# Kernel tuning notes

Hardware: AMD Instinct MI355X
Metric: run time of the kernel (lower is better)

The kernel has to match this reference:

```python
import jax, jax.numpy as jnp
import numpy as np
from jax import lax

# Cl(3,0) Cayley table: W_eff[i, j] = sum_k T[i, j, k] * w[k], signs transcribed
# verbatim from the 64 scatter ops in _cl300_expand_batched.
_TABLE = [
    [(0, 0, 1), (1, 1, 1), (2, 2, 1), (3, 3, 1), (4, 4, -1), (5, 5, -1), (6, 6, -1), (7, 7, -1)],
    [(1, 0, 1), (0, 1, 1), (4, 2, -1), (5, 3, -1), (2, 4, 1), (3, 5, 1), (7, 6, -1), (6, 7, -1)],
    [(2, 0, 1), (4, 1, 1), (0, 2, 1), (6, 3, -1), (1, 4, -1), (7, 5, 1), (3, 6, 1), (5, 7, 1)],
    [(3, 0, 1), (5, 1, 1), (6, 2, 1), (0, 3, 1), (7, 4, -1), (1, 5, -1), (2, 6, -1), (4, 7, -1)],
    [(4, 0, 1), (2, 1, 1), (1, 2, -1), (7, 3, 1), (0, 4, 1), (6, 5, -1), (5, 6, 1), (3, 7, 1)],
    [(5, 0, 1), (3, 1, 1), (7, 2, -1), (1, 3, -1), (6, 4, 1), (0, 5, 1), (4, 6, -1), (2, 7, -1)],
    [(6, 0, 1), (7, 1, 1), (3, 2, 1), (2, 3, -1), (5, 4, -1), (4, 5, 1), (0, 6, 1), (1, 7, 1)],
    [(7, 0, 1), (6, 1, 1), (5, 2, -1), (4, 3, 1), (3, 4, 1), (2, 5, -1), (1, 6, 1), (0, 7, 1)],
]

def _cayley():
    T = np.zeros((8, 8, 8), np.float32)
    for i, row in enumerate(_TABLE):
        for j, k, s in row:
            T[i, j, k] = s
    return jnp.asarray(T)


def setup_inputs() -> dict:
    key = jax.random.key(0)
    k0, k1 = jax.random.split(key, 2)
    B, F, P, G = 16, 8, 4, 32
    state = jax.random.normal(k0, (B, F, 8, G, G, G), jnp.float32)
    all_weights = jax.random.normal(k1, (F, P, 27, 8), jnp.float32) * 0.05
    # mimic _init_weights: zero the center tap, identity-ish on pass 0
    all_weights = all_weights.at[:, :, 26, :].set(0.0).at[:, 0, 26, 0].set(0.8)
    all_biases = jnp.zeros((F, P, 8), jnp.float32)
    field_mix_logits = jnp.tile(jnp.eye(F, dtype=jnp.float32) * 3.0, (P, 1, 1))
    pass_alpha_logit = jnp.full((P,), -1.0, jnp.float32)
    gate_weight = jnp.full((F, 8), 0.1, jnp.float32)
    gate_bias = jnp.full((F, 8), 2.0, jnp.float32)
    return dict(state=state, all_weights=all_weights, all_biases=all_biases,
                field_mix_logits=field_mix_logits, pass_alpha_logit=pass_alpha_logit,
                gate_weight=gate_weight, gate_bias=gate_bias)


def reference(state, all_weights, all_biases, field_mix_logits,
              pass_alpha_logit, gate_weight, gate_bias):
    B, F, _, G, _, _ = state.shape
    P = all_weights.shape[1]
    G3 = G * G * G
    T = _cayley()
    # sparse signed Cayley expansion: [F,P,27,8] -> [F,P,8,8,3,3,3]
    W_eff = jnp.einsum('ijk,fpck->fpijc', T, all_weights).reshape(F, P, 8, 8, 3, 3, 3)
    mix_all = jax.nn.softmax(field_mix_logits, axis=2)  # [P,F,F]
    x = state
    old_state = state
    for p in range(P):
        x_before = x
        Wg = W_eff[:, p].reshape(F * 8, 8, 3, 3, 3)
        bg = all_biases[:, p].reshape(F * 8)
        xf = x.reshape(B, F * 8, G, G, G)
        # causal shifted conv: asymmetric pad (2,0) per spatial dim, grouped by field
        y = lax.conv_general_dilated(
            xf, Wg, window_strides=(1, 1, 1), padding=[(2, 0), (2, 0), (2, 0)],
            dimension_numbers=('NCDHW', 'OIDHW', 'NCDHW'), feature_group_count=F)
        y = jnp.tanh(y + bg[None, :, None, None, None])  # [B,F*8,G,G,G]
        # cross-field mixing (bmm with shared mix matrix)
        xm = jnp.einsum('gf,bfm->bgm', mix_all[p], y.reshape(B, F, 8 * G3))
        x = xm.reshape(B, F, 8, G, G, G)
        alpha = jax.nn.sigmoid(pass_alpha_logit[p])
        x = alpha * x_before + (1.0 - alpha) * x
    gw = gate_weight.reshape(1, F, 8, 1, 1, 1)
    gb = gate_bias.reshape(1, F, 8, 1, 1, 1)
    gate = jax.nn.sigmoid(gw * old_state + gb)
    return gate * old_state + (1.0 - gate) * x
```

## Files before the change

### kernel.cpp

```cpp
#include <hip/hip_runtime.h>
#include <math.h>

#define B_  16
#define F_  8
#define C_  8
#define G_  32
#define G3_ 32768
#define P_  4
#define N_  (B_*F_*C_*G3_)
#define SF_ (C_*G3_)
#define SB_ (F_*SF_)
#define APACK_SZ (P_*F_*9*64*8)

typedef __attribute__((ext_vector_type(8))) short short8v;
typedef __attribute__((ext_vector_type(4))) float f32x4;
typedef unsigned short u16;
typedef unsigned int u32;

__device__ __constant__ int c_k[8][8] = {
  {0,1,2,3,4,5,6,7},
  {1,0,4,5,2,3,7,6},
  {2,4,0,6,1,7,3,5},
  {3,5,6,0,7,1,2,4},
  {4,2,1,7,0,6,5,3},
  {5,3,7,1,6,0,4,2},
  {6,7,3,2,5,4,0,1},
  {7,6,5,4,3,2,1,0}};
__device__ __constant__ float c_s[8][8] = {
  { 1, 1, 1, 1,-1,-1,-1,-1},
  { 1, 1, 1, 1,-1,-1,-1,-1},
  { 1,-1, 1, 1, 1, 1,-1, 1},
  { 1,-1,-1, 1,-1, 1, 1,-1},
  { 1,-1, 1, 1, 1, 1,-1, 1},
  { 1,-1,-1, 1,-1, 1, 1,-1},
  { 1, 1,-1, 1, 1,-1, 1, 1},
  { 1, 1,-1, 1, 1,-1, 1, 1}};

__device__ __forceinline__ float fast_tanh(float v) {
  float e = __expf(2.f * v);
  return 1.f - 2.f / (e + 1.f);
}
__device__ __forceinline__ float fast_sig(float v) {
  return 1.f / (1.f + __expf(-v));
}
__device__ __forceinline__ u32 bf16_rne(float v) {
  u32 u = __float_as_uint(v);
  return (u + 0x7FFFu + ((u >> 16) & 1u)) >> 16;
}
__device__ __forceinline__ u32 pk_bf16(float a, float b) {
  u32 d;
  asm("v_cvt_pk_bf16_f32 %0, %1, %2" : "=v"(d) : "v"(a), "v"(b));
  return d;
}
__device__ __forceinline__ float bl(u32 u) { return __uint_as_float(u << 16); }
__device__ __forceinline__ float bh(u32 u) { return __uint_as_float(u & 0xffff0000u); }
__device__ __forceinline__ float b16f(u16 v) { return __uint_as_float(((u32)v) << 16); }

#define HS(pt) (((pt) + ((pt) >> 2)) & 3)

__global__ void prep_kernel(const float* __restrict__ all_weights,
                            const float* __restrict__ mix_logits,
                            u16* __restrict__ Apack,
                            float* __restrict__ mix) {
  int idx = blockIdx.x * 256 + threadIdx.x;
  if (idx < APACK_SZ) {
    int e = idx & 7;
    int l = (idx >> 3) & 63;
    int rest = idx >> 9;
    int t = rest % 9;
    int fp = rest / 9;
    int f = fp & 7, p = fp >> 3;
    int g = l >> 4, m = l & 15;
    int zoff = m >> 3, i = m & 7;
    int kk = g*4 + (e & 3) + ((e >= 4) ? 16 : 0);
    int zl = kk >> 3, j = kk & 7;
    int dz = zl - zoff;
    float val = 0.f;
    if (dz >= 0 && dz <= 2)
      val = c_s[i][j] * all_weights[((f*P_ + p)*27 + (dz*9 + t))*8 + c_k[i][j]];
    Apack[idx] = (u16)bf16_rne(val);
  }
  if (blockIdx.x == 0 && threadIdx.x < P_*F_) {
    int p = threadIdx.x / F_, g = threadIdx.x % F_;
    const float* row = &mix_logits[(p*F_ + g)*F_];
    float mx = row[0];
    for (int f = 1; f < F_; ++f) mx = fmaxf(mx, row[f]);
    float e[F_]; float sum = 0.f;
    for (int f = 0; f < F_; ++f) { e[f] = __expf(row[f] - mx); sum += e[f]; }
    float inv = 1.f / sum;
    for (int f = 0; f < F_; ++f) mix[(p*F_ + g)*F_ + f] = e[f] * inv;
  }
}

#define RSTG 6
#define TPTS 204

template<int MODE>
__device__ __forceinline__ uint4 field_step(
    int f, const void* __restrict__ xsrc_, const u16* __restrict__ Apack,
    const float* __restrict__ biases, int p, int b, int z0, int y0,
    u32* xk, int tid, int lane, int wid, int g, int ln) {
  if (f) __syncthreads();

  if (tid < 192) {
    int qq  = tid / 48;
    int r2  = tid - qq*48;
    int row = r2 >> 3;
    int c   = r2 & 7;
    int zl = qq >> 1, jq = qq & 1;
    int gz0 = z0 - 2 + zl;
    int gy  = y0 - 2 + row;
    int gx  = c * 4;
    int off = (jq*4)*G3_ + gz0*1024 + gy*32 + gx;
    int ptb = row*34 + 2 + gx;
    u32 d0[4], d1[4], d2[4], d3[4];
    if (MODE != 0) {
      const u16* s0 = (const u16*)xsrc_ + (size_t)b*SB_ + f*SF_ + off;
      const u16* s1 = s0 + 2048;
      uint2 a0={0,0},a1={0,0},a2={0,0},a3={0,0};
      uint2 e0={0,0},e1={0,0},e2={0,0},e3={0,0};
      if (gy >= 0) {
        if (gz0 >= 0) {
          a0 = *(const uint2*)(s0);
          a1 = *(const uint2*)(s0 + G3_);
          a2 = *(const uint2*)(s0 + 2*G3_);
          a3 = *(const uint2*)(s0 + 3*G3_);
        }
        e0 = *(const uint2*)(s1);
        e1 = *(const uint2*)(s1 + G3_);
        e2 = *(const uint2*)(s1 + 2*G3_);
        e3 = *(const uint2*)(s1 + 3*G3_);
      }
      d0[0] = __builtin_amdgcn_perm(a1.x, a0.x, 0x05040100u);
      d0[1] = __builtin_amdgcn_perm(a1.x, a0.x, 0x07060302u);
      d0[2] = __builtin_amdgcn_perm(a1.y, a0.y, 0x05040100u);
      d0[3] = __builtin_amdgcn_perm(a1.y, a0.y, 0x07060302u);
      d1[0] = __builtin_amdgcn_perm(a3.x, a2.x, 0x05040100u);
      d1[1] = __builtin_amdgcn_perm(a3.x, a2.x, 0x07060302u);
      d1[2] = __builtin_amdgcn_perm(a3.y, a2.y, 0x05040100u);
      d1[3] = __builtin_amdgcn_perm(a3.y, a2.y, 0x07060302u);
      d2[0] = __builtin_amdgcn_perm(e1.x, e0.x, 0x05040100u);
      d2[1] = __builtin_amdgcn_perm(e1.x, e0.x, 0x07060302u);
      d2[2] = __builtin_amdgcn_perm(e1.y, e0.y, 0x05040100u);
      d2[3] = __builtin_amdgcn_perm(e1.y, e0.y, 0x07060302u);
      d3[0] = __builtin_amdgcn_perm(e3.x, e2.x, 0x05040100u);
      d3[1] = __builtin_amdgcn_perm(e3.x, e2.x, 0x07060302u);
      d3[2] = __builtin_amdgcn_perm(e3.y, e2.y, 0x05040100u);
      d3[3] = __builtin_amdgcn_perm(e3.y, e2.y, 0x07060302u);
    } else {
      const float* s0 = (const float*)xsrc_ + (size_t)b*SB_ + f*SF_ + off;
      const float* s1 = s0 + 2048;
      float4 A0={0,0,0,0},A1={0,0,0,0},A2={0,0,0,0},A3={0,0,0,0};
      float4 B0={0,0,0,0},B1={0,0,0,0},B2={0,0,0,0},B3={0,0,0,0};
      if (gy >= 0) {
        if (gz0 >= 0) {
          A0 = *(const float4*)(s0);
          A1 = *(const float4*)(s0 + G3_);
          A2 = *(const float4*)(s0 + 2*G3_);
          A3 = *(const float4*)(s0 + 3*G3_);
        }
        B0 = *(const float4*)(s1);
        B1 = *(const float4*)(s1 + G3_);
        B2 = *(const float4*)(s1 + 2*G3_);
        B3 = *(const float4*)(s1 + 3*G3_);
      }
      d0[0]=pk_bf16(A0.x,A1.x); d1[0]=pk_bf16(A2.x,A3.x);
      d2[0]=pk_bf16(B0.x,B1.x); d3[0]=pk_bf16(B2.x,B3.x);
      d0[1]=pk_bf16(A0.y,A1.y); d1[1]=pk_bf16(A2.y,A3.y);
      d2[1]=pk_bf16(B0.y,B1.y); d3[1]=pk_bf16(B2.y,B3.y);
      d0[2]=pk_bf16(A0.z,A1.z); d1[2]=pk_bf16(A2.z,A3.z);
      d2[2]=pk_bf16(B0.z,B1.z); d3[2]=pk_bf16(B2.z,B3.z);
      d0[3]=pk_bf16(A0.w,A1.w); d1[3]=pk_bf16(A2.w,A3.w);
      d2[3]=pk_bf16(B0.w,B1.w); d3[3]=pk_bf16(B2.w,B3.w);
    }
    #define STW(px) { \
      uint4 d; d.x = d0[px]; d.y = d1[px]; d.z = d2[px]; d.w = d3[px]; \
      int pt = ptb + px; \
      *(uint4*)&xk[pt*16 + ((qq ^ HS(pt)) << 2)] = d; }
    STW(0) STW(1) STW(2) STW(3)
    #undef STW
  }

  short8v a[9];
  const u16* ap = Apack + (size_t)((p*8 + f) * 9) * 512;
  #pragma unroll
  for (int t = 0; t < 9; ++t)
    a[t] = *(const short8v*)(ap + (t*64 + lane)*8);

  __syncthreads();

  f32x4 acc0 = {0.f,0.f,0.f,0.f}, acc1 = {0.f,0.f,0.f,0.f};
  #pragma unroll
  for (int dy = 0; dy < 3; ++dy) {
    int prow = (wid + dy)*34;
    #pragma unroll
    for (int dx = 0; dx < 3; ++dx) {
      int t = dy*3 + dx;
      int pt0 = prow + ln + dx;
      int dwb = pt0*16 + ((g ^ HS(pt0)) << 2);
      short8v b0 = *(const short8v*)&xk[dwb];
      short8v b1 = *(const short8v*)&xk[dwb + 256];
      acc0 = __builtin_amdgcn_mfma_f32_16x16x32_bf16(a[t], b0, acc0, 0, 0, 0);
      acc1 = __builtin_amdgcn_mfma_f32_16x16x32_bf16(a[t], b1, acc1, 0, 0, 0);
    }
  }

  const float* bb = biases + (f*P_ + p)*8 + (g & 1)*4;
  float b0v = bb[0], b1v = bb[1], b2v = bb[2], b3v = bb[3];
  uint4 yp;
  yp.x = pk_bf16(fast_tanh(acc0[0] + b0v), fast_tanh(acc0[1] + b1v));
  yp.y = pk_bf16(fast_tanh(acc0[2] + b2v), fast_tanh(acc0[3] + b3v));
  yp.z = pk_bf16(fast_tanh(acc1[0] + b0v), fast_tanh(acc1[1] + b1v));
  yp.w = pk_bf16(fast_tanh(acc1[2] + b2v), fast_tanh(acc1[3] + b3v));
  return yp;
}

template<int MODE>
__global__ __launch_bounds__(256, 4)
void fused_kernel(const void* __restrict__ xsrc_,
                  void* __restrict__ xdst_,
                  const float* __restrict__ state,
                  const u16* __restrict__ Apack,
                  const float* __restrict__ biases,
                  const float* __restrict__ mixb,
                  const float* __restrict__ pal,
                  const float* __restrict__ gw,
                  const float* __restrict__ gb,
                  int p) {
  __shared__ __align__(16) u32 xk[TPTS * 16];

  int bid = blockIdx.x;
  int yt = bid & 7;
  int zt = (bid >> 3) & 15;
  int b  =  bid >> 7;
  int z0 = zt * 2, y0 = yt * 4;
  int tid  = threadIdx.x;
  int lane = tid & 63;
  int wid  = tid >> 6;
  int g    = lane >> 4;
  int ln   = lane & 15;

  if (tid < 192) {
    int pt = (tid >> 5) * 34 + ((tid >> 4) & 1);
    xk[pt*16 + (tid & 15)] = 0u;
  }

  uint4 yp0 = field_step<MODE>(0, xsrc_, Apack, biases, p, b, z0, y0, xk, tid, lane, wid, g, ln);
  uint4 yp1 = field_step<MODE>(1, xsrc_, Apack, biases, p, b, z0, y0, xk, tid, lane, wid, g, ln);
  uint4 yp2 = field_step<MODE>(2, xsrc_, Apack, biases, p, b, z0, y0, xk, tid, lane, wid, g, ln);
  uint4 yp3 = field_step<MODE>(3, xsrc_, Apack, biases, p, b, z0, y0, xk, tid, lane, wid, g, ln);
  uint4 yp4 = field_step<MODE>(4, xsrc_, Apack, biases, p, b, z0, y0, xk, tid, lane, wid, g, ln);
  uint4 yp5 = field_step<MODE>(5, xsrc_, Apack, biases, p, b, z0, y0, xk, tid, lane, wid, g, ln);
  uint4 yp6 = field_step<MODE>(6, xsrc_, Apack, biases, p, b, z0, y0, xk, tid, lane, wid, g, ln);
  uint4 yp7 = field_step<MODE>(7, xsrc_, Apack, biases, p, b, z0, y0, xk, tid, lane, wid, g, ln);

  float yf[8][8];
  #define UNP(F, YPV) \
    yf[F][0]=bl(YPV.x); yf[F][1]=bh(YPV.x); yf[F][2]=bl(YPV.y); yf[F][3]=bh(YPV.y); \
    yf[F][4]=bl(YPV.z); yf[F][5]=bh(YPV.z); yf[F][6]=bl(YPV.w); yf[F][7]=bh(YPV.w);
  UNP(0,yp0) UNP(1,yp1) UNP(2,yp2) UNP(3,yp3)
  UNP(4,yp4) UNP(5,yp5) UNP(6,yp6) UNP(7,yp7)
  #undef UNP

  float alpha = fast_sig(pal[p]);
  float na = 1.f - alpha;
  int zoff = g >> 1;
  int i0 = (g & 1)*4;
  size_t ebase = (size_t)b*SB_ + (size_t)(z0 + zoff)*1024 + (size_t)(y0 + wid)*32 + ln;

  #pragma unroll
  for (int gg = 0; gg < 8; ++gg) {
    const float* mr = mixb + (p*8 + gg)*8;
    float o[8] = {0.f,0.f,0.f,0.f,0.f,0.f,0.f,0.f};
    #pragma unroll
    for (int f = 0; f < 8; ++f) {
      float m = mr[f];
      #pragma unroll
      for (int e = 0; e < 8; ++e) o[e] = fmaf(m, yf[f][e], o[e]);
    }
    size_t obase = ebase + (size_t)gg*SF_;
    #pragma unroll
    for (int e = 0; e < 8; ++e) {
      size_t idx = obase + (size_t)(i0 + (e & 3))*G3_ + (e >> 2)*16;
      float xbv;
      if (MODE == 0) xbv = ((const float*)xsrc_)[idx];
      else           xbv = b16f(((const u16*)xsrc_)[idx]);
      float xf = alpha*xbv + na*o[e];
      if (MODE == 2) {
        float st = state[idx];
        float w = gw[gg*8 + i0 + (e & 3)];
        float bbv = gb[gg*8 + i0 + (e & 3)];
        float gt = fast_sig(w*st + bbv);
        ((float*)xdst_)[idx] = gt*st + (1.f - gt)*xf;
      } else {
        ((u16*)xdst_)[idx] = (u16)bf16_rne(xf);
      }
    }
  }
}

extern "C" void kernel_launch(void* const* d_in, const int* in_sizes, int n_in,
                              void* d_out, int out_size, void* d_ws, size_t ws_size,
                              hipStream_t stream) {
  (void)in_sizes; (void)n_in; (void)out_size; (void)ws_size;
  const float* state       = (const float*)d_in[0];
  const float* all_weights = (const float*)d_in[1];
  const float* all_biases  = (const float*)d_in[2];
  const float* mix_logits  = (const float*)d_in[3];
  const float* pal         = (const float*)d_in[4];
  const float* gw          = (const float*)d_in[5];
  const float* gb          = (const float*)d_in[6];
  float* out = (float*)d_out;

  u16* X0 = (u16*)d_ws;
  u16* X1 = X0 + N_;
  u16* Apack = X1 + N_;
  float* mixb = (float*)(Apack + APACK_SZ);

  prep_kernel<<<dim3(APACK_SZ/256), dim3(256), 0, stream>>>(
      all_weights, mix_logits, Apack, mixb);

  dim3 grid(2048), blk(256);
  fused_kernel<0><<<grid, blk, 0, stream>>>((const void*)state, (void*)X0, state,
      Apack, all_biases, mixb, pal, gw, gb, 0);
  fused_kernel<1><<<grid, blk, 0, stream>>>((const void*)X0, (void*)X1, state,
      Apack, all_biases, mixb, pal, gw, gb, 1);
  fused_kernel<1><<<grid, blk, 0, stream>>>((const void*)X1, (void*)X0, state,
      Apack, all_biases, mixb, pal, gw, gb, 2);
  fused_kernel<2><<<grid, blk, 0, stream>>>((const void*)X0, (void*)out, state,
      Apack, all_biases, mixb, pal, gw, gb, 3);
}
```

Measured before the change: 320.8 us.

## Store intermediate bf16 state channel-interleaved for vector loads and stores

The intermediate bf16 state buffers switch from planar NCDHW layout to a point-major layout with the 8 Clifford channels of a field packed into one 16-byte word. The halo staging in shared memory becomes a single uint4 load per point with no byte permutes, and the epilogue reads and writes 8-byte packed pairs instead of scattered 2-byte elements. The weight packing in the prep kernel is reindexed to match the new K ordering, and the launch bound occupancy hint rises from 4 to 6 blocks per CU. The higher occupancy hint may force register spills.

```diff
diff --git a/kernel.cpp b/kernel.cpp
--- a/kernel.cpp
+++ b/kernel.cpp
@@ -54,7 +54,6 @@
 }
 __device__ __forceinline__ float bl(u32 u) { return __uint_as_float(u << 16); }
 __device__ __forceinline__ float bh(u32 u) { return __uint_as_float(u & 0xffff0000u); }
-__device__ __forceinline__ float b16f(u16 v) { return __uint_as_float(((u32)v) << 16); }
 
 #define HS(pt) (((pt) + ((pt) >> 2)) & 3)
 
@@ -64,7 +63,7 @@
                             float* __restrict__ mix) {
   int idx = blockIdx.x * 256 + threadIdx.x;
   if (idx < APACK_SZ) {
-    int e = idx & 7;
+    int j = idx & 7;
     int l = (idx >> 3) & 63;
     int rest = idx >> 9;
     int t = rest % 9;
@@ -72,9 +71,7 @@
     int f = fp & 7, p = fp >> 3;
     int g = l >> 4, m = l & 15;
     int zoff = m >> 3, i = m & 7;
-    int kk = g*4 + (e & 3) + ((e >= 4) ? 16 : 0);
-    int zl = kk >> 3, j = kk & 7;
-    int dz = zl - zoff;
+    int dz = g - zoff;
     float val = 0.f;
     if (dz >= 0 && dz <= 2)
       val = c_s[i][j] * all_weights[((f*P_ + p)*27 + (dz*9 + t))*8 + c_k[i][j]];
@@ -92,7 +89,6 @@
   }
 }
 
-#define RSTG 6
 #define TPTS 204
 
 template<int MODE>
@@ -102,82 +98,52 @@
     u32* xk, int tid, int lane, int wid, int g, int ln) {
   if (f) __syncthreads();
 
-  if (tid < 192) {
-    int qq  = tid / 48;
-    int r2  = tid - qq*48;
+  if (MODE != 0) {
+    const uint4* xp = (const uint4*)xsrc_ + (size_t)(b*8 + f)*G3_;
+    #pragma unroll
+    for (int it0 = 0; it0 < 3; ++it0) {
+      int it = it0*256 + tid;
+      int gx = it & 31;
+      int pr = it >> 5;
+      int zl = pr / 6;
+      int row = pr - zl*6;
+      int gz = z0 - 2 + zl;
+      int gy = y0 - 2 + row;
+      uint4 v = {0u,0u,0u,0u};
+      if (gz >= 0 && gy >= 0)
+        v = xp[gz*1024 + gy*32 + gx];
+      int pt = row*34 + 2 + gx;
+      *(uint4*)&xk[pt*16 + ((zl ^ HS(pt)) << 2)] = v;
+    }
+  } else if (tid < 192) {
+    int zl  = tid / 48;
+    int r2  = tid - zl*48;
     int row = r2 >> 3;
     int c   = r2 & 7;
-    int zl = qq >> 1, jq = qq & 1;
-    int gz0 = z0 - 2 + zl;
-    int gy  = y0 - 2 + row;
-    int gx  = c * 4;
-    int off = (jq*4)*G3_ + gz0*1024 + gy*32 + gx;
+    int gz = z0 - 2 + zl;
+    int gy = y0 - 2 + row;
+    int gx = c * 4;
+    const float* s0 = (const float*)xsrc_ + (size_t)b*SB_ + f*SF_
+                    + gz*1024 + gy*32 + gx;
+    float4 f0={0,0,0,0},f1={0,0,0,0},f2={0,0,0,0},f3={0,0,0,0};
+    float4 f4={0,0,0,0},f5={0,0,0,0},f6={0,0,0,0},f7={0,0,0,0};
+    if (gz >= 0 && gy >= 0) {
+      f0 = *(const float4*)(s0);
+      f1 = *(const float4*)(s0 + G3_);
+      f2 = *(const float4*)(s0 + 2*G3_);
+      f3 = *(const float4*)(s0 + 3*G3_);
+      f4 = *(const float4*)(s0 + 4*G3_);
+      f5 = *(const float4*)(s0 + 5*G3_);
+      f6 = *(const float4*)(s0 + 6*G3_);
+      f7 = *(const float4*)(s0 + 7*G3_);
+    }
     int ptb = row*34 + 2 + gx;
-    u32 d0[4], d1[4], d2[4], d3[4];
-    if (MODE != 0) {
-      const u16* s0 = (const u16*)xsrc_ + (size_t)b*SB_ + f*SF_ + off;
-      const u16* s1 = s0 + 2048;
-      uint2 a0={0,0},a1={0,0},a2={0,0},a3={0,0};
-      uint2 e0={0,0},e1={0,0},e2={0,0},e3={0,0};
-      if (gy >= 0) {
-        if (gz0 >= 0) {
-          a0 = *(const uint2*)(s0);
-          a1 = *(const uint2*)(s0 + G3_);
-          a2 = *(const uint2*)(s0 + 2*G3_);
-          a3 = *(const uint2*)(s0 + 3*G3_);
-        }
-        e0 = *(const uint2*)(s1);
-        e1 = *(const uint2*)(s1 + G3_);
-        e2 = *(const uint2*)(s1 + 2*G3_);
-        e3 = *(const uint2*)(s1 + 3*G3_);
-      }
-      d0[0] = __builtin_amdgcn_perm(a1.x, a0.x, 0x05040100u);
-      d0[1] = __builtin_amdgcn_perm(a1.x, a0.x, 0x07060302u);
-      d0[2] = __builtin_amdgcn_perm(a1.y, a0.y, 0x05040100u);
-      d0[3] = __builtin_amdgcn_perm(a1.y, a0.y, 0x07060302u);
-      d1[0] = __builtin_amdgcn_perm(a3.x, a2.x, 0x05040100u);
-      d1[1] = __builtin_amdgcn_perm(a3.x, a2.x, 0x07060302u);
-      d1[2] = __builtin_amdgcn_perm(a3.y, a2.y, 0x05040100u);
-      d1[3] = __builtin_amdgcn_perm(a3.y, a2.y, 0x07060302u);
-      d2[0] = __builtin_amdgcn_perm(e1.x, e0.x, 0x05040100u);
-      d2[1] = __builtin_amdgcn_perm(e1.x, e0.x, 0x07060302u);
-      d2[2] = __builtin_amdgcn_perm(e1.y, e0.y, 0x05040100u);
-      d2[3] = __builtin_amdgcn_perm(e1.y, e0.y, 0x07060302u);
-      d3[0] = __builtin_amdgcn_perm(e3.x, e2.x, 0x05040100u);
-      d3[1] = __builtin_amdgcn_perm(e3.x, e2.x, 0x07060302u);
-      d3[2] = __builtin_amdgcn_perm(e3.y, e2.y, 0x05040100u);
-      d3[3] = __builtin_amdgcn_perm(e3.y, e2.y, 0x07060302u);
-    } else {
-      const float* s0 = (const float*)xsrc_ + (size_t)b*SB_ + f*SF_ + off;
-      const float* s1 = s0 + 2048;
-      float4 A0={0,0,0,0},A1={0,0,0,0},A2={0,0,0,0},A3={0,0,0,0};
-      float4 B0={0,0,0,0},B1={0,0,0,0},B2={0,0,0,0},B3={0,0,0,0};
-      if (gy >= 0) {
-        if (gz0 >= 0) {
-          A0 = *(const float4*)(s0);
-          A1 = *(const float4*)(s0 + G3_);
-          A2 = *(const float4*)(s0 + 2*G3_);
-          A3 = *(const float4*)(s0 + 3*G3_);
-        }
-        B0 = *(const float4*)(s1);
-        B1 = *(const float4*)(s1 + G3_);
-        B2 = *(const float4*)(s1 + 2*G3_);
-        B3 = *(const float4*)(s1 + 3*G3_);
-      }
-      d0[0]=pk_bf16(A0.x,A1.x); d1[0]=pk_bf16(A2.x,A3.x);
-      d2[0]=pk_bf16(B0.x,B1.x); d3[0]=pk_bf16(B2.x,B3.x);
-      d0[1]=pk_bf16(A0.y,A1.y); d1[1]=pk_bf16(A2.y,A3.y);
-      d2[1]=pk_bf16(B0.y,B1.y); d3[1]=pk_bf16(B2.y,B3.y);
-      d0[2]=pk_bf16(A0.z,A1.z); d1[2]=pk_bf16(A2.z,A3.z);
-      d2[2]=pk_bf16(B0.z,B1.z); d3[2]=pk_bf16(B2.z,B3.z);
-      d0[3]=pk_bf16(A0.w,A1.w); d1[3]=pk_bf16(A2.w,A3.w);
-      d2[3]=pk_bf16(B0.w,B1.w); d3[3]=pk_bf16(B2.w,B3.w);
-    }
-    #define STW(px) { \
-      uint4 d; d.x = d0[px]; d.y = d1[px]; d.z = d2[px]; d.w = d3[px]; \
+    #define STW(px, CC) { \
+      uint4 d; d.x = pk_bf16(f0.CC, f1.CC); d.y = pk_bf16(f2.CC, f3.CC); \
+      d.z = pk_bf16(f4.CC, f5.CC); d.w = pk_bf16(f6.CC, f7.CC); \
       int pt = ptb + px; \
-      *(uint4*)&xk[pt*16 + ((qq ^ HS(pt)) << 2)] = d; }
-    STW(0) STW(1) STW(2) STW(3)
+      *(uint4*)&xk[pt*16 + ((zl ^ HS(pt)) << 2)] = d; }
+    STW(0, x) STW(1, y) STW(2, z) STW(3, w)
     #undef STW
   }
 
@@ -216,7 +182,7 @@
 }
 
 template<int MODE>
-__global__ __launch_bounds__(256, 4)
+__global__ __launch_bounds__(256, 6)
 void fused_kernel(const void* __restrict__ xsrc_,
                   void* __restrict__ xdst_,
                   const float* __restrict__ state,
@@ -266,7 +232,10 @@
   float na = 1.f - alpha;
   int zoff = g >> 1;
   int i0 = (g & 1)*4;
-  size_t ebase = (size_t)b*SB_ + (size_t)(z0 + zoff)*1024 + (size_t)(y0 + wid)*32 + ln;
+  size_t pt0 = (size_t)(b*8)*G3_ + (size_t)(z0 + zoff)*1024
+             + (size_t)(y0 + wid)*32 + ln;
+  size_t ebase = (size_t)b*SB_ + (size_t)(z0 + zoff)*1024
+               + (size_t)(y0 + wid)*32 + ln;
 
   #pragma unroll
   for (int gg = 0; gg < 8; ++gg) {
@@ -278,23 +247,42 @@
       #pragma unroll
       for (int e = 0; e < 8; ++e) o[e] = fmaf(m, yf[f][e], o[e]);
     }
-    size_t obase = ebase + (size_t)gg*SF_;
-    #pragma unroll
-    for (int e = 0; e < 8; ++e) {
-      size_t idx = obase + (size_t)(i0 + (e & 3))*G3_ + (e >> 2)*16;
-      float xbv;
-      if (MODE == 0) xbv = ((const float*)xsrc_)[idx];
-      else           xbv = b16f(((const u16*)xsrc_)[idx]);
-      float xf = alpha*xbv + na*o[e];
-      if (MODE == 2) {
+    size_t ptg = pt0 + (size_t)gg*G3_;
+    size_t og  = ebase + (size_t)gg*SF_;
+
+    float xb[8];
+    if (MODE == 0) {
+      #pragma unroll
+      for (int e = 0; e < 8; ++e)
+        xb[e] = ((const float*)xsrc_)[og + (size_t)(i0 + (e & 3))*G3_ + (e >> 2)*16];
+    } else {
+      const uint2* xbp = (const uint2*)xsrc_;
+      uint2 u0 = xbp[ptg*2 + (g & 1)];
+      uint2 u1 = xbp[(ptg + 16)*2 + (g & 1)];
+      xb[0]=bl(u0.x); xb[1]=bh(u0.x); xb[2]=bl(u0.y); xb[3]=bh(u0.y);
+      xb[4]=bl(u1.x); xb[5]=bh(u1.x); xb[6]=bl(u1.y); xb[7]=bh(u1.y);
+    }
+
+    if (MODE == 2) {
+      #pragma unroll
+      for (int e = 0; e < 8; ++e) {
+        size_t idx = og + (size_t)(i0 + (e & 3))*G3_ + (e >> 2)*16;
+        float xf = alpha*xb[e] + na*o[e];
         float st = state[idx];
-        float w = gw[gg*8 + i0 + (e & 3)];
-        float bbv = gb[gg*8 + i0 + (e & 3)];
-        float gt = fast_sig(w*st + bbv);
+        float w  = gw[gg*8 + i0 + (e & 3)];
+        float bv = gb[gg*8 + i0 + (e & 3)];
+        float gt = fast_sig(w*st + bv);
         ((float*)xdst_)[idx] = gt*st + (1.f - gt)*xf;
-      } else {
-        ((u16*)xdst_)[idx] = (u16)bf16_rne(xf);
       }
+    } else {
+      uint2* xdp = (uint2*)xdst_;
+      uint2 w0, w1;
+      w0.x = pk_bf16(alpha*xb[0] + na*o[0], alpha*xb[1] + na*o[1]);
+      w0.y = pk_bf16(alpha*xb[2] + na*o[2], alpha*xb[3] + na*o[3]);
+      w1.x = pk_bf16(alpha*xb[4] + na*o[4], alpha*xb[5] + na*o[5]);
+      w1.y = pk_bf16(alpha*xb[6] + na*o[6], alpha*xb[7] + na*o[7]);
+      xdp[ptg*2 + (g & 1)]        = w0;
+      xdp[(ptg + 16)*2 + (g & 1)] = w1;
     }
   }
 }
```

New measurement: 593.0 us. +84.8%, slower.

## Stage epilogue stores through LDS for vectorized writes, remap block order, raise occupancy

Applied to the files above, without the earlier changes.

The epilogue now writes each wave's mixed outputs into a per-wave shared-memory buffer and then emits wide 16-byte global stores, instead of scattered 2- or 4-byte stores per element. Block indices are remapped so consecutive blocks differ in y-tile stride, which changes L2 locality and the order in which CUs work through the tiles. The minimum-blocks hint in launch bounds goes from 4 to 6, which tightens the register budget and may cause spills. The extra LDS buffer adds shared-memory use per block, and the new ordering may help or hurt halo reuse.

```diff
diff --git a/kernel.cpp b/kernel.cpp
--- a/kernel.cpp
+++ b/kernel.cpp
@@ -92,7 +92,6 @@
   }
 }
 
-#define RSTG 6
 #define TPTS 204
 
 template<int MODE>
@@ -216,7 +215,7 @@
 }
 
 template<int MODE>
-__global__ __launch_bounds__(256, 4)
+__global__ __launch_bounds__(256, 6)
 void fused_kernel(const void* __restrict__ xsrc_,
                   void* __restrict__ xdst_,
                   const float* __restrict__ state,
@@ -228,8 +227,10 @@
                   const float* __restrict__ gb,
                   int p) {
   __shared__ __align__(16) u32 xk[TPTS * 16];
-
-  int bid = blockIdx.x;
+  __shared__ __align__(16) u32 obuf[4][576];
+
+  int orig = blockIdx.x;
+  int bid  = (orig & 7) * 256 + (orig >> 3);
   int yt = bid & 7;
   int zt = (bid >> 3) & 15;
   int b  =  bid >> 7;
@@ -268,6 +269,14 @@
   int i0 = (g & 1)*4;
   size_t ebase = (size_t)b*SB_ + (size_t)(z0 + zoff)*1024 + (size_t)(y0 + wid)*32 + ln;
 
+  u16*   ob16 = (u16*)&obuf[wid][0];
+  float* ob32 = (float*)&obuf[wid][0];
+  int srow = lane >> 2;
+  int sc   = srow >> 1, sz = srow & 1;
+  int sx   = (lane & 3) * 8;
+  size_t sbase = (size_t)b*SB_ + (size_t)sc*G3_ + (size_t)(z0 + sz)*1024
+               + (size_t)(y0 + wid)*32 + sx;
+
   #pragma unroll
   for (int gg = 0; gg < 8; ++gg) {
     const float* mr = mixb + (p*8 + gg)*8;
@@ -278,23 +287,43 @@
       #pragma unroll
       for (int e = 0; e < 8; ++e) o[e] = fmaf(m, yf[f][e], o[e]);
     }
-    size_t obase = ebase + (size_t)gg*SF_;
-    #pragma unroll
-    for (int e = 0; e < 8; ++e) {
-      size_t idx = obase + (size_t)(i0 + (e & 3))*G3_ + (e >> 2)*16;
-      float xbv;
-      if (MODE == 0) xbv = ((const float*)xsrc_)[idx];
-      else           xbv = b16f(((const u16*)xsrc_)[idx]);
-      float xf = alpha*xbv + na*o[e];
-      if (MODE == 2) {
+    size_t og = ebase + (size_t)gg*SF_;
+
+    float xb[8];
+    if (MODE == 0) {
+      #pragma unroll
+      for (int e = 0; e < 8; ++e)
+        xb[e] = ((const float*)xsrc_)[og + (size_t)(i0 + (e & 3))*G3_ + ((e >> 2) << 4)];
+    } else {
+      #pragma unroll
+      for (int e = 0; e < 8; ++e)
+        xb[e] = b16f(((const u16*)xsrc_)[og + (size_t)(i0 + (e & 3))*G3_ + ((e >> 2) << 4)]);
+    }
+
+    if (MODE == 2) {
+      #pragma unroll
+      for (int e = 0; e < 8; ++e) {
+        size_t idx = og + (size_t)(i0 + (e & 3))*G3_ + ((e >> 2) << 4);
+        float xf = alpha*xb[e] + na*o[e];
         float st = state[idx];
-        float w = gw[gg*8 + i0 + (e & 3)];
-        float bbv = gb[gg*8 + i0 + (e & 3)];
-        float gt = fast_sig(w*st + bbv);
-        ((float*)xdst_)[idx] = gt*st + (1.f - gt)*xf;
-      } else {
-        ((u16*)xdst_)[idx] = (u16)bf16_rne(xf);
+        float w  = gw[gg*8 + i0 + (e & 3)];
+        float bv = gb[gg*8 + i0 + (e & 3)];
+        float gt = fast_sig(w*st + bv);
+        ob32[((i0 + (e & 3))*2 + zoff)*36 + ln + ((e >> 2) << 4)] = gt*st + (1.f - gt)*xf;
       }
+      float4 v0 = *(const float4*)&ob32[srow*36 + sx];
+      float4 v1 = *(const float4*)&ob32[srow*36 + sx + 4];
+      float* op = (float*)xdst_ + sbase + (size_t)gg*SF_;
+      *(float4*)(op)     = v0;
+      *(float4*)(op + 4) = v1;
+    } else {
+      #pragma unroll
+      for (int e = 0; e < 8; ++e) {
+        float xf = alpha*xb[e] + na*o[e];
+        ob16[((i0 + (e & 3))*2 + zoff)*32 + ln + ((e >> 2) << 4)] = (u16)bf16_rne(xf);
+      }
+      uint4 v = *(const uint4*)&ob16[srow*32 + sx];
+      *(uint4*)((u16*)xdst_ + sbase + (size_t)gg*SF_) = v;
     }
   }
 }
```

After: 843.3 us. 2.63x slower.
